# Kernel optimization log

Measured on AMD Instinct MI355X. Metric: run time of the kernel, lower is better.

## Reference

```python
import jax, jax.numpy as jnp
import numpy as np

B, N, D, Kp = 32, 4096, 128, 256  # batch*heads, seq_len, head_dim, linformer proj dim


def setup_inputs() -> dict:
    key = jax.random.key(0)
    ks = jax.random.split(key, 7)
    return {
        "Q": jax.random.normal(ks[0], (B, N, D), dtype=jnp.float32),
        "K": jax.random.normal(ks[1], (B, N, D), dtype=jnp.float32),
        "V": jax.random.normal(ks[2], (B, N, D), dtype=jnp.float32),
        "E_W": jax.random.normal(ks[3], (Kp, N), dtype=jnp.float32) * (1.0 / np.sqrt(N)),
        "E_b": jax.random.normal(ks[4], (Kp,), dtype=jnp.float32) * 0.02,
        "F_W": jax.random.normal(ks[5], (Kp, N), dtype=jnp.float32) * (1.0 / np.sqrt(N)),
        "F_b": jax.random.normal(ks[6], (Kp,), dtype=jnp.float32) * 0.02,
    }


def reference(Q, K, V, E_W, E_b, F_W, F_b):
    d = Q.shape[-1]
    scale = 1.0 / jnp.sqrt(jnp.asarray(d, Q.dtype))
    # E projection on K^T: [B,d,n] @ W^T -> [B,d,k]
    K_proj = jnp.einsum('bnd,kn->bdk', K, E_W) + E_b  # bias broadcasts over k axis
    # scaled scores [B,n,k], softmax over projected dim k
    scores = jnp.einsum('bnd,bdk->bnk', Q, K_proj) * scale
    P_bar = jax.nn.softmax(scores, axis=-1)
    # F projection on V^T then transpose back: [B,k,d]
    V_proj = jnp.einsum('bnd,kn->bkd', V, F_W) + F_b[:, None]
    # [B,n,k] @ [B,k,d] -> [B,n,d]
    return jnp.einsum('bnk,bkd->bnd', P_bar, V_proj)
```

## Files before the change

kernel.cpp:

```cpp
#include <hip/hip_runtime.h>
#include <cstdint>
#include <cstddef>

#define N_SEQ 4096
#define D_HEAD 128
#define KP_DIM 256

typedef __attribute__((ext_vector_type(4))) float f32x4;
typedef __attribute__((ext_vector_type(8))) short bf16x8;
typedef __attribute__((ext_vector_type(2))) unsigned int u32x2;

static __device__ __forceinline__ short f2bf(float f) {
  uint32_t u = __builtin_bit_cast(uint32_t, f);
  u += 0x7FFFu + ((u >> 16) & 1u);
  return (short)(u >> 16);
}

static __device__ __forceinline__ unsigned int cvtpk(float a, float b) {
  unsigned int r;
  asm("v_cvt_pk_bf16_f32 %0, %1, %2" : "=v"(r) : "v"(a), "v"(b));
  return r;
}

static __device__ __forceinline__ int swz8(int r) { return (r ^ (r >> 2)) & 7; }

__global__ __launch_bounds__(256) void conv_w_kernel(
    const float* __restrict__ EW, const float* __restrict__ FW,
    short* __restrict__ wbf) {
  const int idx = blockIdx.x * 256 + threadIdx.x;
  const int half = 262144;
  f32x4 v = (idx < half) ? *(const f32x4*)(EW + (size_t)idx * 4)
                         : *(const f32x4*)(FW + (size_t)(idx - half) * 4);
  u32x2 h = {cvtpk(v[0], v[1]), cvtpk(v[2], v[3])};
  *(u32x2*)(wbf + (size_t)idx * 4) = h;
}

__global__ __launch_bounds__(512, 4) void proj_partial_kernel(
    const float* __restrict__ Kin, const float* __restrict__ Vin,
    const short* __restrict__ wbf, float* __restrict__ pws) {
  const int bid = blockIdx.x;
  const int wk = (bid & 7) * 64 + (bid >> 3);
  const int dh = wk & 1;
  const int b = (wk >> 1) & 31;
  const int s = (wk >> 6) & 3;
  const int p = wk >> 8;

  const float* __restrict__ X =
      (p == 0 ? Kin : Vin) + (size_t)b * (N_SEQ * D_HEAD) + dh * 64;
  const short* __restrict__ wp = wbf + (size_t)p * (KP_DIM * N_SEQ);
  float* __restrict__ outp = pws + ((((size_t)b * 2 + p) * 4) + s) * (KP_DIM * D_HEAD)
                             + dh * 64;

  __shared__ __align__(16) short lw[2][KP_DIM * 64];
  __shared__ __align__(16) short xt[2][64 * 64];

  const int t = threadIdx.x;
  const int lane = t & 63;
  const int w = t >> 6;
  const int wkk = w * 32;
  const int l15 = lane & 15;
  const int l4 = lane >> 4;
  const int dq = t & 15;
  const int rp = t >> 4;

  const int n0 = s * 1024;

  f32x4 acc[2][4];
#pragma unroll
  for (int i = 0; i < 2; ++i)
#pragma unroll
    for (int j = 0; j < 4; ++j) acc[i][j] = (f32x4){0.f, 0.f, 0.f, 0.f};

  f32x4 xA[2], xB[2];

#define PROJ_WISSUE(BUF, NC)                                                        \
  do {                                                                              \
    _Pragma("unroll") for (int i_ = 0; i_ < 4; ++i_) {                              \
      int g_ = t + i_ * 512;                                                        \
      int row_ = g_ >> 3, c_ = g_ & 7;                                              \
      __builtin_amdgcn_global_load_lds(                                             \
          (const __attribute__((address_space(1))) void*)(wp + (size_t)row_ * N_SEQ \
              + (NC) + ((c_ ^ swz8(row_)) << 3)),                                   \
          (__attribute__((address_space(3))) void*)(&lw[BUF][g_ * 8]), 16, 0, 0);   \
    }                                                                               \
  } while (0)

#define PROJ_XISSUE(XR, NC)                                                         \
  do {                                                                              \
    _Pragma("unroll") for (int i_ = 0; i_ < 2; ++i_)                                \
      XR[i_] = *(const f32x4*)(X + (size_t)((NC) + rp * 2 + i_) * D_HEAD + dq * 4); \
  } while (0)

#define PROJ_XCVT(XR, BUF)                                                          \
  do {                                                                              \
    _Pragma("unroll") for (int j_ = 0; j_ < 4; ++j_) {                              \
      int drow_ = dq * 4 + j_;                                                      \
      unsigned int hv_ = cvtpk(XR[0][j_], XR[1][j_]);                               \
      *(unsigned int*)(&xt[BUF][drow_ * 64 + ((rp * 2) ^ (swz8(drow_) << 3))]) = hv_; \
    }                                                                               \
  } while (0)

#define PROJ_COMPUTE(CUR)                                                           \
  do {                                                                              \
    _Pragma("unroll") for (int ks2 = 0; ks2 < 2; ++ks2) {                           \
      const int col0 = ks2 * 32 + l4 * 8;                                           \
      bf16x8 a_[2], bb_[4];                                                         \
      _Pragma("unroll") for (int mt_ = 0; mt_ < 2; ++mt_) {                         \
        int row_ = wkk + mt_ * 16 + l15;                                            \
        a_[mt_] = *(const bf16x8*)(&lw[CUR][row_ * 64 + (col0 ^ (swz8(row_) << 3))]); \
      }                                                                             \
      _Pragma("unroll") for (int nt_ = 0; nt_ < 4; ++nt_) {                         \
        int row_ = nt_ * 16 + l15;                                                  \
        bb_[nt_] = *(const bf16x8*)(&xt[CUR][row_ * 64 + (col0 ^ (swz8(row_) << 3))]); \
      }                                                                             \
      _Pragma("unroll") for (int mt_ = 0; mt_ < 2; ++mt_)                           \
        _Pragma("unroll") for (int nt_ = 0; nt_ < 4; ++nt_)                         \
          acc[mt_][nt_] = __builtin_amdgcn_mfma_f32_16x16x32_bf16(a_[mt_], bb_[nt_], \
                                                                  acc[mt_][nt_], 0, 0, 0); \
    }                                                                               \
  } while (0)

  PROJ_XISSUE(xA, n0);
  PROJ_WISSUE(0, n0);
  asm volatile("s_waitcnt vmcnt(4)" ::: "memory");
  PROJ_XCVT(xA, 0);
  PROJ_XISSUE(xB, n0 + 64);
  asm volatile("s_waitcnt vmcnt(2)" ::: "memory");
  __syncthreads();

  for (int itp = 0; itp < 7; ++itp) {
    const int it0 = itp * 2;
    PROJ_WISSUE(1, n0 + (it0 + 1) * 64);
    PROJ_XISSUE(xA, n0 + (it0 + 2) * 64);
    PROJ_COMPUTE(0);
    asm volatile("s_waitcnt vmcnt(6)" ::: "memory");
    PROJ_XCVT(xB, 1);
    asm volatile("s_waitcnt vmcnt(2)" ::: "memory");
    __syncthreads();
    PROJ_WISSUE(0, n0 + (it0 + 2) * 64);
    PROJ_XISSUE(xB, n0 + (it0 + 3) * 64);
    PROJ_COMPUTE(1);
    asm volatile("s_waitcnt vmcnt(6)" ::: "memory");
    PROJ_XCVT(xA, 0);
    asm volatile("s_waitcnt vmcnt(2)" ::: "memory");
    __syncthreads();
  }
  PROJ_WISSUE(1, n0 + 15 * 64);
  PROJ_COMPUTE(0);
  asm volatile("s_waitcnt vmcnt(4)" ::: "memory");
  PROJ_XCVT(xB, 1);
  asm volatile("s_waitcnt vmcnt(0)" ::: "memory");
  __syncthreads();
  PROJ_COMPUTE(1);

#undef PROJ_WISSUE
#undef PROJ_XISSUE
#undef PROJ_XCVT
#undef PROJ_COMPUTE

#pragma unroll
  for (int mt = 0; mt < 2; ++mt)
#pragma unroll
    for (int nt = 0; nt < 4; ++nt)
#pragma unroll
      for (int r = 0; r < 4; ++r) {
        int kk = wkk + mt * 16 + l4 * 4 + r;
        int dd = nt * 16 + l15;
        outp[kk * D_HEAD + dd] = acc[mt][nt][r];
      }
}

__global__ __launch_bounds__(256) void reduce_bias_kernel(
    const float* __restrict__ pws, const float* __restrict__ Eb,
    const float* __restrict__ Fb, short* __restrict__ kp, short* __restrict__ vpt) {
  const int sub = blockIdx.x & 3;
  const int b = blockIdx.x >> 2;
  const int t = threadIdx.x;
  __shared__ short tile[128 * 128];
  if (sub < 2) {
    const float* __restrict__ base = pws + ((size_t)b * 2) * 4 * 32768;
    const int off = sub * 16384;
    for (int i = t; i < 16384; i += 256) {
      int ii = off + i;
      int k = ii >> 7;
      float v = base[ii] + base[ii + 32768] + base[ii + 65536] + base[ii + 98304] + Eb[k];
      kp[(size_t)b * 32768 + ii] = f2bf(v);
    }
  } else {
    const int kh = sub - 2;
    const float* __restrict__ base = pws + (((size_t)b * 2 + 1) * 4) * 32768 + kh * 16384;
    for (int i = t; i < 16384; i += 256) {
      int kl = i >> 7, d = i & 127;
      float v = base[i] + base[i + 32768] + base[i + 65536] + base[i + 98304] + Fb[kh * 128 + kl];
      tile[kl * 128 + (d ^ ((kl & 15) << 3))] = f2bf(v);
    }
    __syncthreads();
    for (int i = t; i < 16384; i += 256) {
      int d = i >> 7, kl = i & 127;
      vpt[(size_t)b * 32768 + d * 256 + kh * 128 + kl] = tile[kl * 128 + (d ^ ((kl & 15) << 3))];
    }
  }
}

__global__ __launch_bounds__(1024, 4) void attn_kernel(
    const float* __restrict__ Q, const short* __restrict__ kp,
    const short* __restrict__ vpt, float* __restrict__ out) {
  const int bid = blockIdx.x;
  const int wk = (bid & 7) * 32 + (bid >> 3);
  const int b = wk >> 3;
  const int slice = wk & 7;
  const int t = threadIdx.x;
  const int lane = t & 63;
  const int w = t >> 6;
  const int l15 = lane & 15, l4 = lane >> 4;

  __shared__ __align__(16) short lbuf[81920];
  short* lkp = lbuf;
  short* lvpt = lbuf + 32768;
  short* lpw = lbuf + 65536 + w * 1024;

  const short* __restrict__ kpb = kp + (size_t)b * 32768;
  const short* __restrict__ vptb = vpt + (size_t)b * 32768;

#pragma unroll
  for (int i = 0; i < 4; ++i) {
    int g = t + i * 1024;
    int row = g >> 4, c = g & 15;
    __builtin_amdgcn_global_load_lds(
        (const __attribute__((address_space(1))) void*)(kpb + (size_t)row * 128 +
                                                        ((c ^ (row & 7)) << 3)),
        (__attribute__((address_space(3))) void*)(&lkp[g * 8]), 16, 0, 0);
  }
#pragma unroll
  for (int i = 0; i < 4; ++i) {
    int g = t + i * 1024;
    int row = g >> 5, c = g & 31;
    __builtin_amdgcn_global_load_lds(
        (const __attribute__((address_space(1))) void*)(vptb + (size_t)row * 256 +
                                                        ((c ^ (row & 7)) << 3)),
        (__attribute__((address_space(3))) void*)(&lvpt[g * 8]), 16, 0, 0);
  }

  const float scale = 0.08838834764831845f;
  f32x4 qraw[8];
  {
    const float* qr = Q + ((size_t)b * N_SEQ + slice * 512 + w * 16 + l15) * D_HEAD;
#pragma unroll
    for (int ks = 0; ks < 4; ++ks) {
      qraw[2 * ks] = *(const f32x4*)(qr + ks * 32 + l4 * 8);
      qraw[2 * ks + 1] = *(const f32x4*)(qr + ks * 32 + l4 * 8 + 4);
    }
  }
  asm volatile("s_waitcnt vmcnt(0)" ::: "memory");
  __syncthreads();

#pragma unroll
  for (int rd = 0; rd < 2; ++rd) {
    const int rowBase = slice * 512 + rd * 256 + w * 16;

    bf16x8 qf[4];
#pragma unroll
    for (int ks = 0; ks < 4; ++ks) {
      union { unsigned int u[4]; bf16x8 v; } cv;
      cv.u[0] = cvtpk(qraw[2 * ks][0] * scale, qraw[2 * ks][1] * scale);
      cv.u[1] = cvtpk(qraw[2 * ks][2] * scale, qraw[2 * ks][3] * scale);
      cv.u[2] = cvtpk(qraw[2 * ks + 1][0] * scale, qraw[2 * ks + 1][1] * scale);
      cv.u[3] = cvtpk(qraw[2 * ks + 1][2] * scale, qraw[2 * ks + 1][3] * scale);
      qf[ks] = cv.v;
    }

    f32x4 accs[16];
#pragma unroll
    for (int i = 0; i < 16; ++i) accs[i] = (f32x4){0.f, 0.f, 0.f, 0.f};
#pragma unroll
    for (int ks = 0; ks < 4; ++ks) {
#pragma unroll
      for (int nt = 0; nt < 16; ++nt) {
        bf16x8 af = *(const bf16x8*)(&lkp[(nt * 16 + l15) * 128 +
                                          (((ks * 4 + l4) ^ (l15 & 7)) << 3)]);
        accs[nt] = __builtin_amdgcn_mfma_f32_16x16x32_bf16(af, qf[ks], accs[nt], 0, 0, 0);
      }
    }

    float m = -1e30f;
#pragma unroll
    for (int nt = 0; nt < 16; ++nt)
#pragma unroll
      for (int r = 0; r < 4; ++r) m = fmaxf(m, accs[nt][r]);
    m = fmaxf(m, __shfl_xor(m, 16));
    m = fmaxf(m, __shfl_xor(m, 32));
    float s = 0.f;
#pragma unroll
    for (int nt = 0; nt < 16; ++nt)
#pragma unroll
      for (int r = 0; r < 4; ++r) {
        float e = __expf(accs[nt][r] - m);
        accs[nt][r] = e;
        s += e;
      }
    s += __shfl_xor(s, 16);
    s += __shfl_xor(s, 32);
    float inv = 1.0f / s;

    f32x4 acco[8];
#pragma unroll
    for (int i = 0; i < 8; ++i) acco[i] = (f32x4){0.f, 0.f, 0.f, 0.f};
#pragma unroll
    for (int qq = 0; qq < 4; ++qq) {
#pragma unroll
      for (int ntl = 0; ntl < 4; ++ntl) {
        int nt = qq * 4 + ntl;
        int cw = 2 * ntl + (l4 >> 1);
        unsigned int p0 = cvtpk(accs[nt][0] * inv, accs[nt][1] * inv);
        unsigned int p1 = cvtpk(accs[nt][2] * inv, accs[nt][3] * inv);
        *(u32x2*)((char*)lpw + l15 * 128 + ((cw ^ (l15 & 7)) << 4) + (l4 & 1) * 8) =
            (u32x2){p0, p1};
      }
      if (rd == 0 && qq == 3) {
        const float* qr = Q + ((size_t)b * N_SEQ + slice * 512 + 256 + w * 16 + l15) * D_HEAD;
#pragma unroll
        for (int ks = 0; ks < 4; ++ks) {
          qraw[2 * ks] = *(const f32x4*)(qr + ks * 32 + l4 * 8);
          qraw[2 * ks + 1] = *(const f32x4*)(qr + ks * 32 + l4 * 8 + 4);
        }
      }
#pragma unroll
      for (int ksl = 0; ksl < 2; ++ksl) {
        bf16x8 pa = *(const bf16x8*)((char*)lpw + l15 * 128 +
                                     (((4 * ksl + l4) ^ (l15 & 7)) << 4));
        int ksa = qq * 2 + ksl;
#pragma unroll
        for (int ntv = 0; ntv < 8; ++ntv) {
          bf16x8 av = *(const bf16x8*)(&lvpt[(ntv * 16 + l15) * 256 +
                                             (((ksa * 4 + l4) ^ (l15 & 7)) << 3)]);
          acco[ntv] = __builtin_amdgcn_mfma_f32_16x16x32_bf16(av, pa, acco[ntv], 0, 0, 0);
        }
      }
    }

    float* ob = out + ((size_t)b * N_SEQ + rowBase) * D_HEAD;
#pragma unroll
    for (int ntv = 0; ntv < 8; ++ntv)
      *(f32x4*)(ob + (size_t)l15 * D_HEAD + ntv * 16 + l4 * 4) = acco[ntv];
  }
}

extern "C" void kernel_launch(void* const* d_in, const int* in_sizes, int n_in,
                              void* d_out, int out_size, void* d_ws, size_t ws_size,
                              hipStream_t stream) {
  const float* Q  = (const float*)d_in[0];
  const float* K  = (const float*)d_in[1];
  const float* V  = (const float*)d_in[2];
  const float* EW = (const float*)d_in[3];
  const float* Eb = (const float*)d_in[4];
  const float* FW = (const float*)d_in[5];
  const float* Fb = (const float*)d_in[6];
  float* out = (float*)d_out;

  short* wbf = (short*)d_out;
  float* pws = (float*)d_out + 2097152;
  short* kpb = (short*)d_ws;
  short* vpt = (short*)((char*)d_ws + (size_t)32 * KP_DIM * D_HEAD * 2);

  conv_w_kernel<<<dim3(2048), dim3(256), 0, stream>>>(EW, FW, wbf);
  proj_partial_kernel<<<dim3(512), dim3(512), 0, stream>>>(K, V, wbf, pws);
  reduce_bias_kernel<<<dim3(128), dim3(256), 0, stream>>>(pws, Eb, Fb, kpb, vpt);
  attn_kernel<<<dim3(256), dim3(1024), 0, stream>>>(Q, kpb, vpt, out);
}
```

Before: 95.87 us.

## Fuse split-K reduction and bias into projection kernel via last-block atomic counter

Removes the separate reduce_bias kernel. Each projection block now bumps an atomic counter for its (p, b, dh) group, and the last of the four sequence-split blocks sums the partials, adds the bias, converts to bf16 and writes K_proj, or the transposed V_proj through shared memory. Blocks are remapped so the four splits of a group sit close together in launch order. This saves a kernel launch and its global round-trip scheduling, at the cost of a memset, threadfences and a serial tail done by fewer blocks.

```diff
diff --git a/kernel.cpp b/kernel.cpp
--- a/kernel.cpp
+++ b/kernel.cpp
@@ -37,13 +37,18 @@
 
 __global__ __launch_bounds__(512, 4) void proj_partial_kernel(
     const float* __restrict__ Kin, const float* __restrict__ Vin,
-    const short* __restrict__ wbf, float* __restrict__ pws) {
+    const short* __restrict__ wbf, float* __restrict__ pws,
+    const float* __restrict__ Eb, const float* __restrict__ Fb,
+    short* __restrict__ kp, short* __restrict__ vpt,
+    unsigned int* __restrict__ cnt) {
   const int bid = blockIdx.x;
   const int wk = (bid & 7) * 64 + (bid >> 3);
-  const int dh = wk & 1;
-  const int b = (wk >> 1) & 31;
-  const int s = (wk >> 6) & 3;
-  const int p = wk >> 8;
+  const int g = wk >> 3;
+  const int b = g & 31;
+  const int p = g >> 5;
+  const int inner = wk & 7;
+  const int s = inner & 3;
+  const int dh = inner >> 2;
 
   const float* __restrict__ X =
       (p == 0 ? Kin : Vin) + (size_t)b * (N_SEQ * D_HEAD) + dh * 64;
@@ -53,6 +58,7 @@
 
   __shared__ __align__(16) short lw[2][KP_DIM * 64];
   __shared__ __align__(16) short xt[2][64 * 64];
+  __shared__ int lastFlag;
 
   const int t = threadIdx.x;
   const int lane = t & 63;
@@ -168,36 +174,42 @@
         int dd = nt * 16 + l15;
         outp[kk * D_HEAD + dd] = acc[mt][nt][r];
       }
-}
-
-__global__ __launch_bounds__(256) void reduce_bias_kernel(
-    const float* __restrict__ pws, const float* __restrict__ Eb,
-    const float* __restrict__ Fb, short* __restrict__ kp, short* __restrict__ vpt) {
-  const int sub = blockIdx.x & 3;
-  const int b = blockIdx.x >> 2;
-  const int t = threadIdx.x;
-  __shared__ short tile[128 * 128];
-  if (sub < 2) {
-    const float* __restrict__ base = pws + ((size_t)b * 2) * 4 * 32768;
-    const int off = sub * 16384;
-    for (int i = t; i < 16384; i += 256) {
-      int ii = off + i;
-      int k = ii >> 7;
-      float v = base[ii] + base[ii + 32768] + base[ii + 65536] + base[ii + 98304] + Eb[k];
-      kp[(size_t)b * 32768 + ii] = f2bf(v);
-    }
-  } else {
-    const int kh = sub - 2;
-    const float* __restrict__ base = pws + (((size_t)b * 2 + 1) * 4) * 32768 + kh * 16384;
-    for (int i = t; i < 16384; i += 256) {
-      int kl = i >> 7, d = i & 127;
-      float v = base[i] + base[i + 32768] + base[i + 65536] + base[i + 98304] + Fb[kh * 128 + kl];
-      tile[kl * 128 + (d ^ ((kl & 15) << 3))] = f2bf(v);
-    }
-    __syncthreads();
-    for (int i = t; i < 16384; i += 256) {
-      int d = i >> 7, kl = i & 127;
-      vpt[(size_t)b * 32768 + d * 256 + kh * 128 + kl] = tile[kl * 128 + (d ^ ((kl & 15) << 3))];
+
+  __threadfence();
+  __syncthreads();
+  if (t == 0)
+    lastFlag = (atomicAdd(&cnt[((p * 32 + b) << 1) + dh], 1u) == 3u) ? 1 : 0;
+  __syncthreads();
+  if (lastFlag) {
+    __threadfence();
+    const float* __restrict__ bp =
+        pws + (((size_t)b * 2 + p) * 4) * (KP_DIM * D_HEAD) + dh * 64;
+    if (p == 0) {
+      for (int i = t; i < 16384; i += 512) {
+        int k = i >> 6, dd = i & 63;
+        int o = k * D_HEAD + dd;
+        float v = bp[o] + bp[o + 32768] + bp[o + 65536] + bp[o + 98304] + Eb[k];
+        kp[(size_t)b * 32768 + (size_t)k * D_HEAD + dh * 64 + dd] = f2bf(v);
+      }
+    } else {
+      short* tp = &lw[0][0];
+#pragma unroll
+      for (int kh = 0; kh < 2; ++kh) {
+        __syncthreads();
+        for (int i = t; i < 8192; i += 512) {
+          int kl = i >> 6, dd = i & 63;
+          int k = kh * 128 + kl;
+          int o = k * D_HEAD + dd;
+          float v = bp[o] + bp[o + 32768] + bp[o + 65536] + bp[o + 98304] + Fb[k];
+          tp[kl * 64 + (dd ^ ((kl & 7) << 3))] = f2bf(v);
+        }
+        __syncthreads();
+        for (int i = t; i < 8192; i += 512) {
+          int dd = i >> 7, kl = i & 127;
+          vpt[(size_t)b * 32768 + (size_t)(dh * 64 + dd) * KP_DIM + kh * 128 + kl] =
+              tp[kl * 64 + (dd ^ ((kl & 7) << 3))];
+        }
+      }
     }
   }
 }
@@ -358,12 +370,14 @@
   float* out = (float*)d_out;
 
   short* wbf = (short*)d_out;
+  unsigned int* cnt = (unsigned int*)((char*)d_out + 4 * 1024 * 1024);
   float* pws = (float*)d_out + 2097152;
   short* kpb = (short*)d_ws;
   short* vpt = (short*)((char*)d_ws + (size_t)32 * KP_DIM * D_HEAD * 2);
 
+  hipMemsetAsync(cnt, 0, 512, stream);
   conv_w_kernel<<<dim3(2048), dim3(256), 0, stream>>>(EW, FW, wbf);
-  proj_partial_kernel<<<dim3(512), dim3(512), 0, stream>>>(K, V, wbf, pws);
-  reduce_bias_kernel<<<dim3(128), dim3(256), 0, stream>>>(pws, Eb, Fb, kpb, vpt);
+  proj_partial_kernel<<<dim3(512), dim3(512), 0, stream>>>(K, V, wbf, pws, Eb, Fb,
+                                                           kpb, vpt, cnt);
   attn_kernel<<<dim3(256), dim3(1024), 0, stream>>>(Q, kpb, vpt, out);
 }
```

Result: slower. 267.7 us (+179.2%).
